# Kernel optimization log

Hardware: AMD Instinct MI355X
Metric: run time of the kernel (lower is better)

Reference implementation:

```python
import jax, jax.numpy as jnp
import numpy as np

T = 5            # Newton-Schulz iterations
NORM_GROUPS = 16 # groups along out_channels
EPS = 1e-5


def setup_inputs() -> dict:
    key = jax.random.key(0)
    # conv weight: [out_ch, in_ch, kh, kw]
    weight = jax.random.normal(key, (2048, 1024, 3, 3), dtype=jnp.float32) * 0.05
    return {"weight": weight}


def reference(weight):
    g = NORM_GROUPS
    out_ch = weight.shape[0]
    Z = weight.reshape(g, out_ch // g, -1)                 # [g, n, d]
    Zc = Z - Z.mean(axis=-1, keepdims=True)                # center each row
    S = jnp.einsum('gnd,gmd->gnm', Zc, Zc)                 # [g, n, n] covariance
    n = S.shape[-1]
    eye = jnp.eye(n, dtype=S.dtype)
    S = S + EPS * eye
    norm_S = jnp.sqrt(jnp.sum(S * S, axis=(1, 2), keepdims=True))  # fro norm, [g,1,1]
    S = S / norm_S

    B0 = jnp.broadcast_to(eye, S.shape)                    # B[0] = I

    def body(B, _):
        B3 = B @ B @ B                                     # matrix_power3
        Bn = 1.5 * B - 0.5 * (B3 @ S)                      # baddbmm(1.5, B, -0.5, B^3, S)
        return Bn, None

    Bt, _ = jax.lax.scan(body, B0, None, length=T)
    W = (Bt @ Zc) / jnp.sqrt(norm_S)                       # [g, n, d]
    return W.reshape(weight.shape)
```

## Files before the change

kernel.cpp:

```cpp
#include <hip/hip_runtime.h>


#define G 16
#define NROW 128
#define D 9216
#define OC 2048
#define KSPLIT 18
#define KCHUNK 512
#define EPSV 1e-5f

typedef float f32x16 __attribute__((ext_vector_type(16)));
typedef __bf16 bf16x8 __attribute__((ext_vector_type(8)));

union Frag {
    uint4 q;
    unsigned short s[8];
    bf16x8 v;
};

static __device__ __forceinline__ unsigned short f2bf(float x) {
    union { float f; unsigned int u; } a; a.f = x;
    unsigned int u = a.u;
    unsigned int r = u + 0x7FFFu + ((u >> 16) & 1u);
    return (unsigned short)(r >> 16);
}

static __device__ __forceinline__ float bf2f(unsigned short s) {
    union { unsigned int u; float f; } a; a.u = ((unsigned int)s) << 16;
    return a.f;
}

static __device__ __forceinline__ int swz(int r, int c) {
    return (r << 7) + ((((c >> 3) ^ (r & 15)) << 3) | (c & 7));
}

__global__ __launch_bounds__(256) void k_center(const float* __restrict__ W,
                                                unsigned short* __restrict__ Zc) {
    int row = blockIdx.x;
    int t = threadIdx.x;
    const float4* wp = (const float4*)(W + (size_t)row * D);
    float4 v[9];
    float s = 0.f;
#pragma unroll
    for (int i = 0; i < 9; i++) {
        v[i] = wp[t + i * 256];
        s += v[i].x + v[i].y + v[i].z + v[i].w;
    }
#pragma unroll
    for (int o = 32; o > 0; o >>= 1) s += __shfl_down(s, o, 64);
    __shared__ float ls[4];
    if ((t & 63) == 0) ls[t >> 6] = s;
    __syncthreads();
    float mean = (ls[0] + ls[1] + ls[2] + ls[3]) * (1.0f / 9216.0f);
    ushort4* zp = (ushort4*)(Zc + (size_t)row * D);
#pragma unroll
    for (int i = 0; i < 9; i++) {
        ushort4 o4;
        o4.x = f2bf(v[i].x - mean);
        o4.y = f2bf(v[i].y - mean);
        o4.z = f2bf(v[i].z - mean);
        o4.w = f2bf(v[i].w - mean);
        zp[t + i * 256] = o4;
    }
}

__global__ __launch_bounds__(256) void k_sgemm(const unsigned short* __restrict__ Zc,
                                               float* __restrict__ Spart) {
    __shared__ unsigned short tile[NROW * 128];
    int bid = blockIdx.x;
    int g = bid / KSPLIT, ks = bid % KSPLIT;
    int t = threadIdx.x, lane = t & 63, wave = t >> 6;
    int mq = (wave & 1) * 64, nq = (wave >> 1) * 64;
    int m = lane & 31, h = lane >> 5;

    f32x16 acc[2][2];
#pragma unroll
    for (int i = 0; i < 2; i++)
#pragma unroll
        for (int j = 0; j < 2; j++)
#pragma unroll
            for (int z = 0; z < 16; z++) acc[i][j][z] = 0.f;

    const unsigned short* zg = Zc + (size_t)g * NROW * D + ks * KCHUNK;

    for (int step = 0; step < 4; step++) {
        int dbase = step * 128;
        __syncthreads();
#pragma unroll
        for (int p = 0; p < 8; p++) {
            int flat = p * 256 + t;
            int r = flat >> 4, gc = flat & 15;
            uint4 dd = *(const uint4*)(zg + (size_t)r * D + dbase + gc * 8);
            *(uint4*)(tile + swz(r, gc * 8)) = dd;
        }
        __syncthreads();
#pragma unroll
        for (int kk = 0; kk < 8; kk++) {
            int kb = kk * 16 + h * 8;
            Frag a0, a1, b0, b1;
            a0.q = *(const uint4*)(tile + swz(mq + m, kb));
            a1.q = *(const uint4*)(tile + swz(mq + 32 + m, kb));
            b0.q = *(const uint4*)(tile + swz(nq + m, kb));
            b1.q = *(const uint4*)(tile + swz(nq + 32 + m, kb));
            acc[0][0] = __builtin_amdgcn_mfma_f32_32x32x16_bf16(a0.v, b0.v, acc[0][0], 0, 0, 0);
            acc[0][1] = __builtin_amdgcn_mfma_f32_32x32x16_bf16(a0.v, b1.v, acc[0][1], 0, 0, 0);
            acc[1][0] = __builtin_amdgcn_mfma_f32_32x32x16_bf16(a1.v, b0.v, acc[1][0], 0, 0, 0);
            acc[1][1] = __builtin_amdgcn_mfma_f32_32x32x16_bf16(a1.v, b1.v, acc[1][1], 0, 0, 0);
        }
    }
    float* sp = Spart + (size_t)(g * KSPLIT + ks) * 16384;
#pragma unroll
    for (int i = 0; i < 2; i++)
#pragma unroll
        for (int j = 0; j < 2; j++)
#pragma unroll
            for (int reg = 0; reg < 16; reg++) {
                int row = (reg & 3) + 8 * (reg >> 2) + 4 * h;
                sp[(mq + i * 32 + row) * 128 + nq + j * 32 + m] = acc[i][j][reg];
            }
}

__global__ __launch_bounds__(256) void k_reduce(const float* __restrict__ Spart,
                                                float* __restrict__ Sred,
                                                float* __restrict__ normAcc) {
    int b = blockIdx.x;
    int g = b >> 4, part = b & 15;
    int el = part * 1024 + threadIdx.x * 4;
    float4 s = {0.f, 0.f, 0.f, 0.f};
    for (int ks = 0; ks < KSPLIT; ks++) {
        float4 p = *(const float4*)(Spart + (size_t)(g * KSPLIT + ks) * 16384 + el);
        s.x += p.x; s.y += p.y; s.z += p.z; s.w += p.w;
    }
    int r = el >> 7, c = el & 127;
    if (r >= c && r <= c + 3) {
        if (r == c) s.x += EPSV;
        else if (r == c + 1) s.y += EPSV;
        else if (r == c + 2) s.z += EPSV;
        else s.w += EPSV;
    }
    *(float4*)(Sred + (size_t)g * 16384 + el) = s;
    float sq = s.x * s.x + s.y * s.y + s.z * s.z + s.w * s.w;
#pragma unroll
    for (int o = 32; o > 0; o >>= 1) sq += __shfl_down(sq, o, 64);
    __shared__ float ls[4];
    if ((threadIdx.x & 63) == 0) ls[threadIdx.x >> 6] = sq;
    __syncthreads();
    if (threadIdx.x == 0) atomicAdd(normAcc + g, ls[0] + ls[1] + ls[2] + ls[3]);
}

__global__ __launch_bounds__(512) void k_ns(const float* __restrict__ Sred,
                                            const float* __restrict__ normAcc,
                                            unsigned short* __restrict__ Bt) {
    extern __shared__ unsigned short sm[];
    unsigned short* Bb = sm;
    unsigned short* Sb = sm + 16384;
    unsigned short* Ub = sm + 32768;
    unsigned short* Vt = sm + 49152;
    int g = blockIdx.x;
    int t = threadIdx.x, lane = t & 63, wave = t >> 6;
    int m = lane & 31, h = lane >> 5;
    float rn = 1.0f / sqrtf(normAcc[g]);

    {
        int r = t >> 2, c0 = (t & 3) * 32;
        const float* sp = Sred + (size_t)g * 16384 + r * 128 + c0;
#pragma unroll
        for (int q = 0; q < 4; q++) {
            int c = c0 + q * 8;
            float4 x0 = *(const float4*)(sp + q * 8);
            float4 x1 = *(const float4*)(sp + q * 8 + 4);
            float vv[8] = {x0.x, x0.y, x0.z, x0.w, x1.x, x1.y, x1.z, x1.w};
            Frag fs, fb;
#pragma unroll
            for (int i = 0; i < 8; i++) {
                float sv = vv[i] * rn;
                fs.s[i] = f2bf(sv);
                float bv = -0.5f * sv + ((r == c + i) ? 1.5f : 0.f);
                fb.s[i] = f2bf(bv);
            }
            *(uint4*)(Sb + swz(r, c)) = fs.q;
            *(uint4*)(Bb + swz(r, c)) = fb.q;
        }
    }
    __syncthreads();

    for (int iter = 0; iter < 4; iter++) {
#pragma unroll
        for (int i = 0; i < 4; i++) {
            int task = wave * 4 + i;
            int tmb = ((task >> 2) & 3) * 32, tnb = (task & 3) * 32;
            const unsigned short* Bsrc = (task < 16) ? Bb : Sb;
            unsigned short* dst = (task < 16) ? Ub : Vt;
            f32x16 acc;
#pragma unroll
            for (int z = 0; z < 16; z++) acc[z] = 0.f;
#pragma unroll
            for (int kk = 0; kk < 8; kk++) {
                Frag a, bfr;
                a.q = *(const uint4*)(Bb + swz(tmb + m, kk * 16 + h * 8));
                bfr.q = *(const uint4*)(Bsrc + swz(tnb + m, kk * 16 + h * 8));
                acc = __builtin_amdgcn_mfma_f32_32x32x16_bf16(a.v, bfr.v, acc, 0, 0, 0);
            }
#pragma unroll
            for (int q = 0; q < 4; q++) {
                union { unsigned short s[4]; uint2 u; } pk;
#pragma unroll
                for (int j = 0; j < 4; j++) pk.s[j] = f2bf(acc[q * 4 + j]);
                int rr = tmb + q * 8 + h * 4;
                int cc = tnb + m;
                *(uint2*)(dst + swz(cc, rr)) = pk.u;
            }
        }
        __syncthreads();
#pragma unroll
        for (int i = 0; i < 2; i++) {
            int task = wave * 2 + i;
            int tmb = (task >> 2) * 32, tnb = (task & 3) * 32;
            f32x16 acc;
#pragma unroll
            for (int z = 0; z < 16; z++) acc[z] = 0.f;
#pragma unroll
            for (int kk = 0; kk < 8; kk++) {
                Frag a, bfr;
                a.q = *(const uint4*)(Ub + swz(tmb + m, kk * 16 + h * 8));
                bfr.q = *(const uint4*)(Vt + swz(tnb + m, kk * 16 + h * 8));
                acc = __builtin_amdgcn_mfma_f32_32x32x16_bf16(a.v, bfr.v, acc, 0, 0, 0);
            }
#pragma unroll
            for (int reg = 0; reg < 16; reg++) {
                int rr = tmb + (reg & 3) + 8 * (reg >> 2) + 4 * h;
                int cc = tnb + m;
                int e = swz(rr, cc);
                Bb[e] = f2bf(1.5f * bf2f(Bb[e]) - 0.5f * acc[reg]);
            }
        }
        __syncthreads();
    }
    {
        int r = t >> 2, c0 = (t & 3) * 32;
        unsigned short* bp = Bt + (size_t)g * 16384 + r * 128;
#pragma unroll
        for (int q = 0; q < 4; q++) {
            uint4 dd = *(const uint4*)(Bb + swz(r, c0 + q * 8));
            *(uint4*)(bp + c0 + q * 8) = dd;
        }
    }
}

__global__ __launch_bounds__(256) void k_wgemm(const unsigned short* __restrict__ Zc,
                                               const unsigned short* __restrict__ Bt,
                                               const float* __restrict__ normAcc,
                                               float* __restrict__ out) {
    __shared__ unsigned short Ab[16384];
    __shared__ unsigned short Zt[16384];
    int nt = blockIdx.x, g = blockIdx.y;
    int t = threadIdx.x, lane = t & 63, wave = t >> 6;
    int m = lane & 31, h = lane >> 5;

    const unsigned short* bg = Bt + (size_t)g * 16384;
    const unsigned short* zg = Zc + (size_t)g * NROW * D + nt * 128;
#pragma unroll
    for (int p = 0; p < 8; p++) {
        int flat = p * 256 + t;
        int r = flat >> 4, gc = flat & 15;
        uint4 da = *(const uint4*)(bg + r * 128 + gc * 8);
        uint4 dz = *(const uint4*)(zg + (size_t)r * D + gc * 8);
        *(uint4*)(Ab + swz(r, gc * 8)) = da;
        *(uint4*)(Zt + swz(r, gc * 8)) = dz;
    }
    __syncthreads();
    float ss = 1.0f / sqrtf(sqrtf(normAcc[g]));

    int cw = wave * 32 + m;

    f32x16 acc[4];
#pragma unroll
    for (int i = 0; i < 4; i++)
#pragma unroll
        for (int z = 0; z < 16; z++) acc[i][z] = 0.f;

#pragma unroll
    for (int ks = 0; ks < 8; ks++) {
        int k0 = ks * 16 + h * 8;
        Frag b;
#pragma unroll
        for (int j = 0; j < 8; j++) b.s[j] = Zt[swz(k0 + j, cw)];
#pragma unroll
        for (int i = 0; i < 4; i++) {
            Frag a;
            a.q = *(const uint4*)(Ab + swz(i * 32 + m, k0));
            acc[i] = __builtin_amdgcn_mfma_f32_32x32x16_bf16(a.v, b.v, acc[i], 0, 0, 0);
        }
    }
    float* og = out + (size_t)(g * NROW) * D + nt * 128 + cw;
#pragma unroll
    for (int i = 0; i < 4; i++)
#pragma unroll
        for (int reg = 0; reg < 16; reg++) {
            int row = i * 32 + (reg & 3) + 8 * (reg >> 2) + 4 * h;
            og[(size_t)row * D] = acc[i][reg] * ss;
        }
}

extern "C" void kernel_launch(void* const* d_in, const int* in_sizes, int n_in,
                              void* d_out, int out_size, void* d_ws, size_t ws_size,
                              hipStream_t stream) {
    const float* W = (const float*)d_in[0];
    float* out = (float*)d_out;
    char* ws = (char*)d_ws;

    unsigned short* Zc = (unsigned short*)(ws);
    float* Spart = (float*)(ws + 37748736ULL);
    float* Sred = (float*)(ws + 56623104ULL);
    float* normAcc = (float*)(ws + 57671680ULL);
    unsigned short* Bt = (unsigned short*)(ws + 57671744ULL);

    k_center<<<OC, 256, 0, stream>>>(W, Zc);
    k_sgemm<<<G * KSPLIT, 256, 0, stream>>>(Zc, Spart);
    hipMemsetAsync(normAcc, 0, 64, stream);
    k_reduce<<<256, 256, 0, stream>>>(Spart, Sred, normAcc);
    hipFuncSetAttribute((const void*)k_ns,
                        hipFuncAttributeMaxDynamicSharedMemorySize, 131072);
    k_ns<<<G, 512, 131072, stream>>>(Sred, normAcc, Bt);
    k_wgemm<<<dim3(72, G), 256, 0, stream>>>(Zc, Bt, normAcc, out);
}
```

Before: 191.5 us.

## Prefetch S-GEMM tiles, drop norm memset/atomics, fold NS update into MFMA

The covariance GEMM now prefetches the next global tile into registers while computing on the current one, and uses 16 K-splits of 576 columns, ending with a half-width step. The Frobenius norm is stored as per-block partials and summed by the consumers, which removes the memset and the atomics. In the Newton-Schulz loop, the 1.5*B - 0.5*B^3 S update is computed by pre-scaling V by -0.5 and adding 1.5*B through extra MFMAs against a scaled identity fragment, replacing a scalar read-modify-write on LDS. This adds an extra barrier and two extra MFMAs per tile in exchange.

```diff
diff --git a/kernel.cpp b/kernel.cpp
--- a/kernel.cpp
+++ b/kernel.cpp
@@ -5,8 +5,8 @@
 #define NROW 128
 #define D 9216
 #define OC 2048
-#define KSPLIT 18
-#define KCHUNK 512
+#define KSPLIT 16
+#define KCHUNK 576
 #define EPSV 1e-5f
 
 typedef float f32x16 __attribute__((ext_vector_type(16)));
@@ -23,11 +23,6 @@
     unsigned int u = a.u;
     unsigned int r = u + 0x7FFFu + ((u >> 16) & 1u);
     return (unsigned short)(r >> 16);
-}
-
-static __device__ __forceinline__ float bf2f(unsigned short s) {
-    union { unsigned int u; float f; } a; a.u = ((unsigned int)s) << 16;
-    return a.f;
 }
 
 static __device__ __forceinline__ int swz(int r, int c) {
@@ -83,19 +78,47 @@
 
     const unsigned short* zg = Zc + (size_t)g * NROW * D + ks * KCHUNK;
 
-    for (int step = 0; step < 4; step++) {
-        int dbase = step * 128;
-        __syncthreads();
-#pragma unroll
-        for (int p = 0; p < 8; p++) {
-            int flat = p * 256 + t;
-            int r = flat >> 4, gc = flat & 15;
-            uint4 dd = *(const uint4*)(zg + (size_t)r * D + dbase + gc * 8);
-            *(uint4*)(tile + swz(r, gc * 8)) = dd;
-        }
-        __syncthreads();
+    uint4 pf[8];
+#pragma unroll
+    for (int p = 0; p < 8; p++) {
+        int flat = p * 256 + t, r = flat >> 4, gc = flat & 15;
+        pf[p] = *(const uint4*)(zg + (size_t)r * D + gc * 8);
+    }
+
+    for (int step = 0; step < 5; step++) {
+        __syncthreads();
+        if (step < 4) {
+#pragma unroll
+            for (int p = 0; p < 8; p++) {
+                int flat = p * 256 + t, r = flat >> 4, gc = flat & 15;
+                *(uint4*)(tile + swz(r, gc * 8)) = pf[p];
+            }
+        } else {
+#pragma unroll
+            for (int p = 0; p < 4; p++) {
+                int flat = p * 256 + t, r = flat >> 3, gc = flat & 7;
+                *(uint4*)(tile + swz(r, gc * 8)) = pf[p];
+            }
+        }
+        __syncthreads();
+        if (step < 3) {
+            int dbase = (step + 1) * 128;
+#pragma unroll
+            for (int p = 0; p < 8; p++) {
+                int flat = p * 256 + t, r = flat >> 4, gc = flat & 15;
+                pf[p] = *(const uint4*)(zg + (size_t)r * D + dbase + gc * 8);
+            }
+        } else if (step == 3) {
+#pragma unroll
+            for (int p = 0; p < 4; p++) {
+                int flat = p * 256 + t, r = flat >> 3, gc = flat & 7;
+                pf[p] = *(const uint4*)(zg + (size_t)r * D + 512 + gc * 8);
+            }
+        }
+        int kmax = (step < 4) ? 8 : 4;
 #pragma unroll
         for (int kk = 0; kk < 8; kk++) {
+            if (kk >= kmax) break;
             int kb = kk * 16 + h * 8;
             Frag a0, a1, b0, b1;
             a0.q = *(const uint4*)(tile + swz(mq + m, kb));
@@ -122,7 +145,7 @@
 
 __global__ __launch_bounds__(256) void k_reduce(const float* __restrict__ Spart,
                                                 float* __restrict__ Sred,
-                                                float* __restrict__ normAcc) {
+                                                float* __restrict__ normPart) {
     int b = blockIdx.x;
     int g = b >> 4, part = b & 15;
     int el = part * 1024 + threadIdx.x * 4;
@@ -145,11 +168,11 @@
     __shared__ float ls[4];
     if ((threadIdx.x & 63) == 0) ls[threadIdx.x >> 6] = sq;
     __syncthreads();
-    if (threadIdx.x == 0) atomicAdd(normAcc + g, ls[0] + ls[1] + ls[2] + ls[3]);
+    if (threadIdx.x == 0) normPart[b] = ls[0] + ls[1] + ls[2] + ls[3];
 }
 
 __global__ __launch_bounds__(512) void k_ns(const float* __restrict__ Sred,
-                                            const float* __restrict__ normAcc,
+                                            const float* __restrict__ normPart,
                                             unsigned short* __restrict__ Bt) {
     extern __shared__ unsigned short sm[];
     unsigned short* Bb = sm;
@@ -159,7 +182,11 @@
     int g = blockIdx.x;
     int t = threadIdx.x, lane = t & 63, wave = t >> 6;
     int m = lane & 31, h = lane >> 5;
-    float rn = 1.0f / sqrtf(normAcc[g]);
+
+    float ns = 0.f;
+#pragma unroll
+    for (int i = 0; i < 16; i++) ns += normPart[g * 16 + i];
+    float rn = 1.0f / sqrtf(ns);
 
     {
         int r = t >> 2, c0 = (t & 3) * 32;
@@ -182,6 +209,14 @@
             *(uint4*)(Bb + swz(r, c)) = fb.q;
         }
     }
+
+    Frag fI[2];
+#pragma unroll
+    for (int kk2 = 0; kk2 < 2; kk2++)
+#pragma unroll
+        for (int j = 0; j < 8; j++)
+            fI[kk2].s[j] = (m == kk2 * 16 + h * 8 + j) ? (unsigned short)0x3FC0 : (unsigned short)0;
+
     __syncthreads();
 
     for (int iter = 0; iter < 4; iter++) {
@@ -191,6 +226,7 @@
             int tmb = ((task >> 2) & 3) * 32, tnb = (task & 3) * 32;
             const unsigned short* Bsrc = (task < 16) ? Bb : Sb;
             unsigned short* dst = (task < 16) ? Ub : Vt;
+            float sc = (task < 16) ? 1.0f : -0.5f;
             f32x16 acc;
 #pragma unroll
             for (int z = 0; z < 16; z++) acc[z] = 0.f;
@@ -205,33 +241,43 @@
             for (int q = 0; q < 4; q++) {
                 union { unsigned short s[4]; uint2 u; } pk;
 #pragma unroll
-                for (int j = 0; j < 4; j++) pk.s[j] = f2bf(acc[q * 4 + j]);
-                int rr = tmb + q * 8 + h * 4;
-                int cc = tnb + m;
-                *(uint2*)(dst + swz(cc, rr)) = pk.u;
-            }
-        }
-        __syncthreads();
+                for (int j = 0; j < 4; j++) pk.s[j] = f2bf(sc * acc[q * 4 + j]);
+                *(uint2*)(dst + swz(tnb + m, tmb + q * 8 + h * 4)) = pk.u;
+            }
+        }
+        __syncthreads();
+        f32x16 acc2[2];
 #pragma unroll
         for (int i = 0; i < 2; i++) {
             int task = wave * 2 + i;
             int tmb = (task >> 2) * 32, tnb = (task & 3) * 32;
-            f32x16 acc;
-#pragma unroll
-            for (int z = 0; z < 16; z++) acc[z] = 0.f;
+#pragma unroll
+            for (int z = 0; z < 16; z++) acc2[i][z] = 0.f;
 #pragma unroll
             for (int kk = 0; kk < 8; kk++) {
                 Frag a, bfr;
                 a.q = *(const uint4*)(Ub + swz(tmb + m, kk * 16 + h * 8));
                 bfr.q = *(const uint4*)(Vt + swz(tnb + m, kk * 16 + h * 8));
-                acc = __builtin_amdgcn_mfma_f32_32x32x16_bf16(a.v, bfr.v, acc, 0, 0, 0);
-            }
-#pragma unroll
-            for (int reg = 0; reg < 16; reg++) {
-                int rr = tmb + (reg & 3) + 8 * (reg >> 2) + 4 * h;
-                int cc = tnb + m;
-                int e = swz(rr, cc);
-                Bb[e] = f2bf(1.5f * bf2f(Bb[e]) - 0.5f * acc[reg]);
+                acc2[i] = __builtin_amdgcn_mfma_f32_32x32x16_bf16(a.v, bfr.v, acc2[i], 0, 0, 0);
+            }
+#pragma unroll
+            for (int kk2 = 0; kk2 < 2; kk2++) {
+                Frag bfr;
+                bfr.q = *(const uint4*)(Bb + swz(tnb + m, tmb + kk2 * 16 + h * 8));
+                acc2[i] = __builtin_amdgcn_mfma_f32_32x32x16_bf16(fI[kk2].v, bfr.v, acc2[i], 0, 0, 0);
+            }
+        }
+        __syncthreads();
+#pragma unroll
+        for (int i = 0; i < 2; i++) {
+            int task = wave * 2 + i;
+            int tmb = (task >> 2) * 32, tnb = (task & 3) * 32;
+#pragma unroll
+            for (int q = 0; q < 4; q++) {
+                union { unsigned short s[4]; uint2 u; } pk;
+#pragma unroll
+                for (int j = 0; j < 4; j++) pk.s[j] = f2bf(acc2[i][q * 4 + j]);
+                *(uint2*)(Bb + swz(tnb + m, tmb + q * 8 + h * 4)) = pk.u;
             }
         }
         __syncthreads();
@@ -249,7 +295,7 @@
 
 __global__ __launch_bounds__(256) void k_wgemm(const unsigned short* __restrict__ Zc,
                                                const unsigned short* __restrict__ Bt,
-                                               const float* __restrict__ normAcc,
+                                               const float* __restrict__ normPart,
                                                float* __restrict__ out) {
     __shared__ unsigned short Ab[16384];
     __shared__ unsigned short Zt[16384];
@@ -269,7 +315,10 @@
         *(uint4*)(Zt + swz(r, gc * 8)) = dz;
     }
     __syncthreads();
-    float ss = 1.0f / sqrtf(sqrtf(normAcc[g]));
+    float nsum = 0.f;
+#pragma unroll
+    for (int i = 0; i < 16; i++) nsum += normPart[g * 16 + i];
+    float ss = 1.0f / sqrtf(sqrtf(nsum));
 
     int cw = wave * 32 + m;
 
@@ -311,16 +360,15 @@
 
     unsigned short* Zc = (unsigned short*)(ws);
     float* Spart = (float*)(ws + 37748736ULL);
-    float* Sred = (float*)(ws + 56623104ULL);
-    float* normAcc = (float*)(ws + 57671680ULL);
-    unsigned short* Bt = (unsigned short*)(ws + 57671744ULL);
+    float* Sred = (float*)(ws + 54525952ULL);
+    float* normPart = (float*)(ws + 55574528ULL);
+    unsigned short* Bt = (unsigned short*)(ws + 55575552ULL);
 
     k_center<<<OC, 256, 0, stream>>>(W, Zc);
     k_sgemm<<<G * KSPLIT, 256, 0, stream>>>(Zc, Spart);
-    hipMemsetAsync(normAcc, 0, 64, stream);
-    k_reduce<<<256, 256, 0, stream>>>(Spart, Sred, normAcc);
+    k_reduce<<<256, 256, 0, stream>>>(Spart, Sred, normPart);
     hipFuncSetAttribute((const void*)k_ns,
                         hipFuncAttributeMaxDynamicSharedMemorySize, 131072);
-    k_ns<<<G, 512, 131072, stream>>>(Sred, normAcc, Bt);
-    k_wgemm<<<dim3(72, G), 256, 0, stream>>>(Zc, Bt, normAcc, out);
-}
+    k_ns<<<G, 512, 131072, stream>>>(Sred, normPart, Bt);
+    k_wgemm<<<dim3(72, G), 256, 0, stream>>>(Zc, Bt, normPart, out);
+}
```

Result: no change. 190.3 us (-0.6%).
